# Performance work log

Hardware: AMD Instinct MI355X
Metric: run time of the kernel (lower is better)

## Reference

```python
import jax, jax.numpy as jnp
import numpy as np


def setup_inputs() -> dict:
    key = jax.random.key(0)
    ks = jax.random.split(key, 8)
    B, L, H, D = 128, 2048, 512, 512
    return {
        "batch": jax.random.normal(ks[0], (B, D), jnp.float32),
        "hid_states": jax.random.normal(ks[1], (B, L, H), jnp.float32),
        "h0": 0.1 * jax.random.normal(ks[2], (B, H), jnp.float32),
        "s0": 0.1 * jax.random.normal(ks[3], (B, H), jnp.float32),
        "W_ih": jax.random.normal(ks[4], (D, 4 * H), jnp.float32) * (1.0 / np.sqrt(D)),
        "W_hh": jax.random.normal(ks[5], (H, 4 * H), jnp.float32) * (1.0 / np.sqrt(H)),
        "b_lstm": jnp.zeros((4 * H,), jnp.float32),
        "W1": jax.random.normal(ks[6], (H, 64), jnp.float32) * (1.0 / np.sqrt(H)),
        "b1": jnp.zeros((64,), jnp.float32),
        "W2": jax.random.normal(ks[7], (64, D), jnp.float32) * (1.0 / np.sqrt(64)),
        "b2": jnp.zeros((D,), jnp.float32),
        "max_len": 10,
    }


def reference(batch, hid_states, h0, s0, W_ih, W_hh, b_lstm, W1, b1, W2, b2, max_len):
    B, D = batch.shape
    eps = 1e-8
    hs_sq = jnp.sum(hid_states * hid_states, axis=2)  # (B, L), loop-invariant

    def step(carry, _):
        x, h, s = carry
        # cosine-similarity attention of state s over recorded hidden states
        num = jnp.einsum('bh,blh->bl', s, hid_states)
        denom = jnp.sqrt(hs_sq * jnp.sum(s * s, axis=1, keepdims=True)) + eps
        energy = jax.nn.softmax(num / denom, axis=1)          # (B, L)
        context = jnp.einsum('blh,bl->bh', hid_states, energy)
        s = s + context
        # LSTM cell step (i, f, g, o gate order)
        gates = x @ W_ih + h @ W_hh + b_lstm
        i, f, g, o = jnp.split(gates, 4, axis=1)
        c = jax.nn.sigmoid(f) * s + jax.nn.sigmoid(i) * jnp.tanh(g)
        h = jax.nn.sigmoid(o) * jnp.tanh(c)
        # 2-layer MLP head produces next input
        x = jax.nn.leaky_relu(h @ W1 + b1, 0.01) @ W2 + b2
        return (x, h, c), x

    (_, _, _), outs = jax.lax.scan(step, (batch, h0, s0), None, length=max_len)
    # replicate torch: cat(dim=1) -> view(B, D, L) -> permute(0, 2, 1)
    flat = jnp.transpose(outs, (1, 0, 2)).reshape(B, max_len * D)
    return flat.reshape(B, D, max_len).transpose(0, 2, 1)
```

## Files before the change

### kernel.cpp

```cpp
#include <hip/hip_runtime.h>
#include <math.h>

#define B 128
#define L 2048
#define H 512
#define D 512
#define NG 2048
#define T 10
#define S 16
#define GB 256

#define OFF_S    ((size_t)0)
#define OFF_H    ((size_t)65536)
#define OFF_X    ((size_t)131072)
#define OFF_SS   ((size_t)196608)
#define OFF_G    ((size_t)196736)
#define OFF_PL   ((size_t)460928)
#define OFF_PCTX ((size_t)462976)
#define OFF_RN   ((size_t)1511552)
#define OFF_HB   ((size_t)1773696)

__device__ __forceinline__ float sigf(float x){ return 1.0f / (1.0f + __expf(-x)); }

__device__ __forceinline__ unsigned int b16r(float f){
    unsigned int u = __float_as_uint(f);
    return (u + 0x7FFFu + ((u >> 16) & 1u)) >> 16;
}
__device__ __forceinline__ unsigned int pack2(float lo, float hi){
    return b16r(lo) | (b16r(hi) << 16);
}

#define UNPK(u, f0, f1) { f0 = __uint_as_float((u) << 16); f1 = __uint_as_float((u) & 0xFFFF0000u); }

__device__ __forceinline__ float block_sum256(float v){
    for (int off = 32; off; off >>= 1) v += __shfl_xor(v, off, 64);
    __shared__ float r[4];
    int wave = threadIdx.x >> 6, lane = threadIdx.x & 63;
    if (lane == 0) r[wave] = v;
    __syncthreads();
    return r[0] + r[1] + r[2] + r[3];
}

__global__ void init_k(const float* __restrict__ s0, const float* __restrict__ h0,
                       const float* __restrict__ x0, float* __restrict__ ws){
    int b = blockIdx.x, t = threadIdx.x;
    float ssq = 0.f;
    for (int h = t; h < H; h += 256){
        float sv = s0[b*H + h];
        ws[OFF_S + b*H + h] = sv;
        ws[OFF_H + b*H + h] = h0[b*H + h];
        ssq += sv * sv;
    }
    for (int d = t; d < D; d += 256) ws[OFF_X + b*D + d] = x0[b*D + d];
    float tot = block_sum256(ssq);
    if (t == 0) ws[OFF_SS + b] = tot;
}

__device__ __forceinline__ void load_snorm(const float* __restrict__ ws, int b, int g, float* sf){
    const float* sb = ws + OFF_S + (size_t)b * H + g * 8;
    float rssb = rsqrtf(ws[OFF_SS + b]);
    #pragma unroll
    for (int cb = 0; cb < 4; cb++){
        float4 a = *(const float4*)(sb + cb*128);
        float4 c = *(const float4*)(sb + cb*128 + 4);
        sf[cb*8+0]=a.x*rssb; sf[cb*8+1]=a.y*rssb; sf[cb*8+2]=a.z*rssb; sf[cb*8+3]=a.w*rssb;
        sf[cb*8+4]=c.x*rssb; sf[cb*8+5]=c.y*rssb; sf[cb*8+6]=c.z*rssb; sf[cb*8+7]=c.w*rssb;
    }
}

__device__ __forceinline__ void attn_epilogue(float* ctx, float lsum, float* smem,
                                              float* __restrict__ ws, int b, int chunk,
                                              int wave, int g, int r){
    #pragma unroll
    for (int k = 0; k < 32; k++){
        ctx[k] += __shfl_xor(ctx[k], 16, 64);
        ctx[k] += __shfl_xor(ctx[k], 32, 64);
    }
    lsum += __shfl_xor(lsum, 16, 64);
    lsum += __shfl_xor(lsum, 32, 64);

    float (*lctx)[512] = (float(*)[512])smem;
    float* ll = smem + 2048;
    if (r == 0){
        #pragma unroll
        for (int cb = 0; cb < 4; cb++){
            float4 a = { ctx[cb*8+0], ctx[cb*8+1], ctx[cb*8+2], ctx[cb*8+3] };
            float4 c = { ctx[cb*8+4], ctx[cb*8+5], ctx[cb*8+6], ctx[cb*8+7] };
            *(float4*)&lctx[wave][cb*128 + g*8]     = a;
            *(float4*)&lctx[wave][cb*128 + g*8 + 4] = c;
        }
        if (g == 0) ll[wave] = lsum;
    }
    __syncthreads();
    int t = threadIdx.x;
    float* pc = ws + OFF_PCTX + ((size_t)b * S + chunk) * H;
    pc[t]       = lctx[0][t]     + lctx[1][t]     + lctx[2][t]     + lctx[3][t];
    pc[t + 256] = lctx[0][t+256] + lctx[1][t+256] + lctx[2][t+256] + lctx[3][t+256];
    if (t == 0) ws[OFF_PL + b*S + chunk] = ll[0] + ll[1] + ll[2] + ll[3];
}

__device__ __forceinline__ void attn_first_body(const float* __restrict__ hid,
                                                float* __restrict__ ws, int bid, float* smem){
    int b = bid >> 4, chunk = bid & (S - 1);
    int wave = threadIdx.x >> 6, lane = threadIdx.x & 63;
    int g = lane & 15, r = lane >> 4;
    float sf[32];
    load_snorm(ws, b, g, sf);

    int l0w = chunk * 128 + wave * 32;
    const float* hsrc = hid + ((size_t)b * L + l0w) * H + g * 8;
    uint4* hbdst = (uint4*)(ws + OFF_HB) + ((size_t)b * L + l0w) * 64 + g;
    float* rnw = ws + OFF_RN + (size_t)b * L + l0w;

    float ctx[32];
    #pragma unroll
    for (int k = 0; k < 32; k++) ctx[k] = 0.f;
    float lsum = 0.f;

    for (int it = 0; it < 8; it++){
        int ro = it*4 + r;
        const float* src = hsrc + (size_t)ro * H;
        float f[32];
        #pragma unroll
        for (int cb = 0; cb < 4; cb++){
            float4 a = *(const float4*)(src + cb*128);
            float4 c = *(const float4*)(src + cb*128 + 4);
            f[cb*8+0]=a.x; f[cb*8+1]=a.y; f[cb*8+2]=a.z; f[cb*8+3]=a.w;
            f[cb*8+4]=c.x; f[cb*8+5]=c.y; f[cb*8+6]=c.z; f[cb*8+7]=c.w;
        }
        float sq = 0.f, dot = 0.f;
        #pragma unroll
        for (int k = 0; k < 32; k++){ sq += f[k]*f[k]; dot += f[k]*sf[k]; }
        sq  += __shfl_xor(sq, 1, 64);  sq  += __shfl_xor(sq, 2, 64);
        sq  += __shfl_xor(sq, 4, 64);  sq  += __shfl_xor(sq, 8, 64);
        dot += __shfl_xor(dot, 1, 64); dot += __shfl_xor(dot, 2, 64);
        dot += __shfl_xor(dot, 4, 64); dot += __shfl_xor(dot, 8, 64);
        float rnv = rsqrtf(sq);
        if (g == 0) rnw[ro] = rnv;
        uint4* drow = hbdst + (size_t)ro * 64;
        #pragma unroll
        for (int cb = 0; cb < 4; cb++){
            uint4 o;
            o.x = pack2(f[cb*8+0], f[cb*8+1]);
            o.y = pack2(f[cb*8+2], f[cb*8+3]);
            o.z = pack2(f[cb*8+4], f[cb*8+5]);
            o.w = pack2(f[cb*8+6], f[cb*8+7]);
            drow[cb*16] = o;
        }
        float p = __expf(dot * rnv);
        lsum += p;
        #pragma unroll
        for (int k = 0; k < 32; k++) ctx[k] += p * f[k];
    }
    attn_epilogue(ctx, lsum, smem, ws, b, chunk, wave, g, r);
}

__device__ __forceinline__ void attn_steady_body(float* __restrict__ ws, int bid, float* smem){
    int b = bid >> 4, chunk = bid & (S - 1);
    int wave = threadIdx.x >> 6, lane = threadIdx.x & 63;
    int g = lane & 15, r = lane >> 4;
    float sf[32];
    load_snorm(ws, b, g, sf);

    int l0w = chunk * 128 + wave * 32;
    const uint4* hbu = (const uint4*)(ws + OFF_HB) + ((size_t)b * L + l0w) * 64 + g;
    const float* rnp = ws + OFF_RN + (size_t)b * L + l0w;

    float ctx[32];
    #pragma unroll
    for (int k = 0; k < 32; k++) ctx[k] = 0.f;
    float lsum = 0.f;

    for (int it = 0; it < 8; it++){
        int ro = it*4 + r;
        const uint4* hr = hbu + (size_t)ro * 64;
        uint4 u0 = hr[0];
        uint4 u1 = hr[16];
        uint4 u2 = hr[32];
        uint4 u3 = hr[48];
        float rnv = rnp[ro];
        float f[32];
        UNPK(u0.x, f[0], f[1])   UNPK(u0.y, f[2], f[3])
        UNPK(u0.z, f[4], f[5])   UNPK(u0.w, f[6], f[7])
        UNPK(u1.x, f[8], f[9])   UNPK(u1.y, f[10], f[11])
        UNPK(u1.z, f[12], f[13]) UNPK(u1.w, f[14], f[15])
        UNPK(u2.x, f[16], f[17]) UNPK(u2.y, f[18], f[19])
        UNPK(u2.z, f[20], f[21]) UNPK(u2.w, f[22], f[23])
        UNPK(u3.x, f[24], f[25]) UNPK(u3.y, f[26], f[27])
        UNPK(u3.z, f[28], f[29]) UNPK(u3.w, f[30], f[31])
        float dot = 0.f;
        #pragma unroll
        for (int k = 0; k < 32; k++) dot += f[k] * sf[k];
        dot += __shfl_xor(dot, 1, 64);
        dot += __shfl_xor(dot, 2, 64);
        dot += __shfl_xor(dot, 4, 64);
        dot += __shfl_xor(dot, 8, 64);
        float p = __expf(dot * rnv);
        lsum += p;
        #pragma unroll
        for (int k = 0; k < 32; k++) ctx[k] += p * f[k];
    }
    attn_epilogue(ctx, lsum, smem, ws, b, chunk, wave, g, r);
}

__device__ __forceinline__ void gates_body(const float* __restrict__ Wih,
                                           const float* __restrict__ Whh,
                                           const float* __restrict__ bias,
                                           float* __restrict__ ws,
                                           float* smem, int gid){
    int tid = threadIdx.x;
    int b0 = (gid >> 4) * 8, n0 = (gid & 15) * 128;
    float* xs  = smem;
    float* hsm = smem + 4096;
    {
        int r = tid >> 5, c = (tid & 31) * 16;
        const float* xsrc = ws + OFF_X + (size_t)(b0 + r) * D + c;
        const float* hsrc = ws + OFF_H + (size_t)(b0 + r) * H + c;
        #pragma unroll
        for (int j = 0; j < 4; j++){
            *(float4*)&xs[r*512 + c + j*4]  = *(const float4*)(xsrc + j*4);
            *(float4*)&hsm[r*512 + c + j*4] = *(const float4*)(hsrc + j*4);
        }
    }
    __syncthreads();
    int nt = tid & 31, kh = tid >> 5;
    int n = n0 + nt * 4;
    float4 acc[8];
    #pragma unroll
    for (int bi = 0; bi < 8; bi++){ acc[bi].x = 0.f; acc[bi].y = 0.f; acc[bi].z = 0.f; acc[bi].w = 0.f; }
    const float* w1p = Wih + (size_t)(kh * 64) * NG + n;
    const float* w2p = Whh + (size_t)(kh * 64) * NG + n;
    const float* xk = xs  + kh * 64;
    const float* hk = hsm + kh * 64;
    #pragma unroll 2
    for (int k = 0; k < 64; k++){
        float4 w1 = *(const float4*)(w1p + (size_t)k * NG);
        float4 w2 = *(const float4*)(w2p + (size_t)k * NG);
        #pragma unroll
        for (int bi = 0; bi < 8; bi++){
            float xv = xk[bi*512 + k], hv = hk[bi*512 + k];
            acc[bi].x += xv*w1.x + hv*w2.x;
            acc[bi].y += xv*w1.y + hv*w2.y;
            acc[bi].z += xv*w1.z + hv*w2.z;
            acc[bi].w += xv*w1.w + hv*w2.w;
        }
    }
    __syncthreads();
    float4* red = (float4*)smem;
    #pragma unroll
    for (int bi = 0; bi < 8; bi++) red[(kh*8 + bi)*32 + nt] = acc[bi];
    __syncthreads();
    int bi2 = tid >> 5, nt2 = tid & 31;
    int n2 = n0 + nt2 * 4;
    float4 s = *(const float4*)(bias + n2);
    #pragma unroll
    for (int k2 = 0; k2 < 8; k2++){
        float4 p = red[(k2*8 + bi2)*32 + nt2];
        s.x += p.x; s.y += p.y; s.z += p.z; s.w += p.w;
    }
    *(float4*)(ws + OFF_G + (size_t)(b0 + bi2)*NG + n2) = s;
}

__global__ __launch_bounds__(256, 3) void fused0_k(const float* __restrict__ hid,
                                                   const float* __restrict__ Wih,
                                                   const float* __restrict__ Whh,
                                                   const float* __restrict__ bias,
                                                   float* __restrict__ ws){
    __shared__ float smem[8192];
    if (blockIdx.x < GB){ gates_body(Wih, Whh, bias, ws, smem, blockIdx.x); return; }
    attn_first_body(hid, ws, blockIdx.x - GB, smem);
}

__global__ __launch_bounds__(256, 3) void fusedN_k(const float* __restrict__ Wih,
                                                   const float* __restrict__ Whh,
                                                   const float* __restrict__ bias,
                                                   float* __restrict__ ws){
    __shared__ float smem[8192];
    if (blockIdx.x < GB){ gates_body(Wih, Whh, bias, ws, smem, blockIdx.x); return; }
    attn_steady_body(ws, blockIdx.x - GB, smem);
}

__global__ __launch_bounds__(512) void tail_k(const float* __restrict__ W1, const float* __restrict__ b1,
                                              const float* __restrict__ W2, const float* __restrict__ b2,
                                              float* __restrict__ ws, float* __restrict__ out, int st){
    int b = blockIdx.x, t = threadIdx.x;
    __shared__ float hl[512];
    __shared__ float part[8][64];
    __shared__ float t1[64];
    __shared__ float rr[8];

    float Ls = 0.f;
    #pragma unroll
    for (int i = 0; i < S; i++) Ls += ws[OFF_PL + b*S + i];
    float inv = 1.0f / Ls;

    float cx = 0.f;
    #pragma unroll
    for (int i = 0; i < S; i++) cx += ws[OFF_PCTX + ((size_t)b*S + i)*H + t];
    const float* g = ws + OFF_G + (size_t)b * NG;
    float sn = ws[OFF_S + b*H + t] + cx * inv;
    float gi = g[t], gf = g[512 + t], gg = g[1024 + t], go = g[1536 + t];
    float c  = sigf(gf) * sn + sigf(gi) * tanhf(gg);
    float hv = sigf(go) * tanhf(c);
    ws[OFF_S + b*H + t] = c;
    ws[OFF_H + b*H + t] = hv;
    hl[t] = hv;
    float csq = c * c;
    for (int off = 32; off; off >>= 1) csq += __shfl_xor(csq, off, 64);
    int wv = t >> 6, ln = t & 63;
    if (ln == 0) rr[wv] = csq;
    __syncthreads();
    if (t == 0){
        float s = 0.f;
        #pragma unroll
        for (int i = 0; i < 8; i++) s += rr[i];
        ws[OFF_SS + b] = s;
    }

    int j = t & 63, q = t >> 6;
    float a = 0.f;
    #pragma unroll 4
    for (int k = q*64; k < q*64 + 64; k++) a += hl[k] * W1[k*64 + j];
    part[q][j] = a;
    __syncthreads();
    if (t < 64){
        float v = b1[t];
        #pragma unroll
        for (int i = 0; i < 8; i++) v += part[i][t];
        t1[t] = v > 0.f ? v : 0.01f * v;
    }
    __syncthreads();
    float a2 = b2[t];
    #pragma unroll
    for (int k = 0; k < 64; k++) a2 += t1[k] * W2[k*512 + t];
    ws[OFF_X + (size_t)b*D + t] = a2;
    int idx = st * D + t;
    out[(size_t)b * (D*T) + (size_t)(idx % T) * D + (idx / T)] = a2;
}

extern "C" void kernel_launch(void* const* d_in, const int* in_sizes, int n_in,
                              void* d_out, int out_size, void* d_ws, size_t ws_size,
                              hipStream_t stream) {
    const float* batch = (const float*)d_in[0];
    const float* hid   = (const float*)d_in[1];
    const float* h0    = (const float*)d_in[2];
    const float* s0    = (const float*)d_in[3];
    const float* Wih   = (const float*)d_in[4];
    const float* Whh   = (const float*)d_in[5];
    const float* bl    = (const float*)d_in[6];
    const float* W1    = (const float*)d_in[7];
    const float* b1    = (const float*)d_in[8];
    const float* W2    = (const float*)d_in[9];
    const float* b2    = (const float*)d_in[10];
    float* out = (float*)d_out;
    float* ws  = (float*)d_ws;

    init_k<<<B, 256, 0, stream>>>(s0, h0, batch, ws);
    fused0_k<<<B*S + GB, 256, 0, stream>>>(hid, Wih, Whh, bl, ws);
    tail_k<<<B, 512, 0, stream>>>(W1, b1, W2, b2, ws, out, 0);
    for (int st = 1; st < T; st++){
        fusedN_k<<<B*S + GB, 256, 0, stream>>>(Wih, Whh, bl, ws);
        tail_k<<<B, 512, 0, stream>>>(W1, b1, W2, b2, ws, out, st);
    }
}
```

Baseline: 1.419 ms.

## Remove init kernel, remap attention lanes to 32-wide rows with register prefetch

The separate init kernel is removed: step 0 reads s0, h0 and batch directly and computes the s-norm inside each attention block, while the tail kernel takes a pointer to the previous s. The attention loops now use 32 lanes per row with 16 elements each, so two rows are in flight per wave instead of four. The loops are fully unrolled with next-row prefetch into registers. Launch bounds are raised to 4 blocks per SM to increase occupancy, which adds register pressure from the prefetch buffers.

```diff
diff --git a/kernel.cpp b/kernel.cpp
--- a/kernel.cpp
+++ b/kernel.cpp
@@ -32,180 +32,193 @@
 
 #define UNPK(u, f0, f1) { f0 = __uint_as_float((u) << 16); f1 = __uint_as_float((u) & 0xFFFF0000u); }
 
-__device__ __forceinline__ float block_sum256(float v){
+__device__ __forceinline__ float red32(float v){
+    v += __shfl_xor(v, 1, 64);
+    v += __shfl_xor(v, 2, 64);
+    v += __shfl_xor(v, 4, 64);
+    v += __shfl_xor(v, 8, 64);
+    v += __shfl_xor(v, 16, 64);
+    return v;
+}
+
+__device__ __forceinline__ float block_sum256s(float v, float* r4){
     for (int off = 32; off; off >>= 1) v += __shfl_xor(v, off, 64);
-    __shared__ float r[4];
     int wave = threadIdx.x >> 6, lane = threadIdx.x & 63;
-    if (lane == 0) r[wave] = v;
-    __syncthreads();
-    return r[0] + r[1] + r[2] + r[3];
-}
-
-__global__ void init_k(const float* __restrict__ s0, const float* __restrict__ h0,
-                       const float* __restrict__ x0, float* __restrict__ ws){
-    int b = blockIdx.x, t = threadIdx.x;
-    float ssq = 0.f;
-    for (int h = t; h < H; h += 256){
-        float sv = s0[b*H + h];
-        ws[OFF_S + b*H + h] = sv;
-        ws[OFF_H + b*H + h] = h0[b*H + h];
-        ssq += sv * sv;
-    }
-    for (int d = t; d < D; d += 256) ws[OFF_X + b*D + d] = x0[b*D + d];
-    float tot = block_sum256(ssq);
-    if (t == 0) ws[OFF_SS + b] = tot;
-}
-
-__device__ __forceinline__ void load_snorm(const float* __restrict__ ws, int b, int g, float* sf){
-    const float* sb = ws + OFF_S + (size_t)b * H + g * 8;
-    float rssb = rsqrtf(ws[OFF_SS + b]);
-    #pragma unroll
-    for (int cb = 0; cb < 4; cb++){
-        float4 a = *(const float4*)(sb + cb*128);
-        float4 c = *(const float4*)(sb + cb*128 + 4);
-        sf[cb*8+0]=a.x*rssb; sf[cb*8+1]=a.y*rssb; sf[cb*8+2]=a.z*rssb; sf[cb*8+3]=a.w*rssb;
-        sf[cb*8+4]=c.x*rssb; sf[cb*8+5]=c.y*rssb; sf[cb*8+6]=c.z*rssb; sf[cb*8+7]=c.w*rssb;
-    }
-}
-
-__device__ __forceinline__ void attn_epilogue(float* ctx, float lsum, float* smem,
-                                              float* __restrict__ ws, int b, int chunk,
-                                              int wave, int g, int r){
-    #pragma unroll
-    for (int k = 0; k < 32; k++){
-        ctx[k] += __shfl_xor(ctx[k], 16, 64);
-        ctx[k] += __shfl_xor(ctx[k], 32, 64);
-    }
-    lsum += __shfl_xor(lsum, 16, 64);
+    if (lane == 0) r4[wave] = v;
+    __syncthreads();
+    return r4[0] + r4[1] + r4[2] + r4[3];
+}
+
+__device__ __forceinline__ void load_snorm16(const float* sptr, float rssb, int g2, float* sf){
+    const float* sb = sptr + g2 * 16;
+    #pragma unroll
+    for (int q = 0; q < 4; q++){
+        float4 a = *(const float4*)(sb + q*4);
+        sf[q*4+0] = a.x * rssb; sf[q*4+1] = a.y * rssb;
+        sf[q*4+2] = a.z * rssb; sf[q*4+3] = a.w * rssb;
+    }
+}
+
+__device__ __forceinline__ void attn_epilogue32(float* ctx, float lsum, float* smem,
+                                                float* __restrict__ pl, float* __restrict__ pc,
+                                                int wave, int g2, int lane){
+    #pragma unroll
+    for (int k = 0; k < 16; k++) ctx[k] += __shfl_xor(ctx[k], 32, 64);
     lsum += __shfl_xor(lsum, 32, 64);
 
     float (*lctx)[512] = (float(*)[512])smem;
     float* ll = smem + 2048;
-    if (r == 0){
-        #pragma unroll
-        for (int cb = 0; cb < 4; cb++){
-            float4 a = { ctx[cb*8+0], ctx[cb*8+1], ctx[cb*8+2], ctx[cb*8+3] };
-            float4 c = { ctx[cb*8+4], ctx[cb*8+5], ctx[cb*8+6], ctx[cb*8+7] };
-            *(float4*)&lctx[wave][cb*128 + g*8]     = a;
-            *(float4*)&lctx[wave][cb*128 + g*8 + 4] = c;
-        }
-        if (g == 0) ll[wave] = lsum;
+    if (lane < 32){
+        #pragma unroll
+        for (int q = 0; q < 4; q++){
+            float4 v = { ctx[q*4+0], ctx[q*4+1], ctx[q*4+2], ctx[q*4+3] };
+            *(float4*)&lctx[wave][g2*16 + q*4] = v;
+        }
+        if (g2 == 0) ll[wave] = lsum;
     }
     __syncthreads();
     int t = threadIdx.x;
-    float* pc = ws + OFF_PCTX + ((size_t)b * S + chunk) * H;
     pc[t]       = lctx[0][t]     + lctx[1][t]     + lctx[2][t]     + lctx[3][t];
     pc[t + 256] = lctx[0][t+256] + lctx[1][t+256] + lctx[2][t+256] + lctx[3][t+256];
-    if (t == 0) ws[OFF_PL + b*S + chunk] = ll[0] + ll[1] + ll[2] + ll[3];
+    if (t == 0) pl[0] = ll[0] + ll[1] + ll[2] + ll[3];
 }
 
 __device__ __forceinline__ void attn_first_body(const float* __restrict__ hid,
-                                                float* __restrict__ ws, int bid, float* smem){
-    int b = bid >> 4, chunk = bid & (S - 1);
+                                                const float* __restrict__ sptr, float rssb,
+                                                float* __restrict__ ws, float* smem,
+                                                float* __restrict__ pl, float* __restrict__ pc,
+                                                int b, int chunk){
     int wave = threadIdx.x >> 6, lane = threadIdx.x & 63;
-    int g = lane & 15, r = lane >> 4;
-    float sf[32];
-    load_snorm(ws, b, g, sf);
+    int g2 = lane & 31, r2 = lane >> 5;
+    float sf[16];
+    load_snorm16(sptr, rssb, g2, sf);
 
     int l0w = chunk * 128 + wave * 32;
-    const float* hsrc = hid + ((size_t)b * L + l0w) * H + g * 8;
-    uint4* hbdst = (uint4*)(ws + OFF_HB) + ((size_t)b * L + l0w) * 64 + g;
+    const float* hsrc = hid + ((size_t)b * L + l0w) * H + g2 * 16;
+    uint4* hbw = (uint4*)(ws + OFF_HB) + ((size_t)b * L + l0w) * 64 + g2 * 2;
     float* rnw = ws + OFF_RN + (size_t)b * L + l0w;
 
-    float ctx[32];
-    #pragma unroll
-    for (int k = 0; k < 32; k++) ctx[k] = 0.f;
+    float ctx[16];
+    #pragma unroll
+    for (int k = 0; k < 16; k++) ctx[k] = 0.f;
     float lsum = 0.f;
 
-    for (int it = 0; it < 8; it++){
-        int ro = it*4 + r;
-        const float* src = hsrc + (size_t)ro * H;
-        float f[32];
-        #pragma unroll
-        for (int cb = 0; cb < 4; cb++){
-            float4 a = *(const float4*)(src + cb*128);
-            float4 c = *(const float4*)(src + cb*128 + 4);
-            f[cb*8+0]=a.x; f[cb*8+1]=a.y; f[cb*8+2]=a.z; f[cb*8+3]=a.w;
-            f[cb*8+4]=c.x; f[cb*8+5]=c.y; f[cb*8+6]=c.z; f[cb*8+7]=c.w;
-        }
-        float sq = 0.f, dot = 0.f;
-        #pragma unroll
-        for (int k = 0; k < 32; k++){ sq += f[k]*f[k]; dot += f[k]*sf[k]; }
-        sq  += __shfl_xor(sq, 1, 64);  sq  += __shfl_xor(sq, 2, 64);
-        sq  += __shfl_xor(sq, 4, 64);  sq  += __shfl_xor(sq, 8, 64);
-        dot += __shfl_xor(dot, 1, 64); dot += __shfl_xor(dot, 2, 64);
-        dot += __shfl_xor(dot, 4, 64); dot += __shfl_xor(dot, 8, 64);
+    const float* s0p = hsrc + (size_t)r2 * H;
+    float4 x0 = *(const float4*)(s0p);
+    float4 x1 = *(const float4*)(s0p + 4);
+    float4 x2 = *(const float4*)(s0p + 8);
+    float4 x3 = *(const float4*)(s0p + 12);
+
+    #pragma unroll
+    for (int it = 0; it < 16; it++){
+        int ro = it*2 + r2;
+        float4 y0, y1, y2, y3;
+        if (it < 15){
+            const float* sn = hsrc + (size_t)(ro + 2) * H;
+            y0 = *(const float4*)(sn);
+            y1 = *(const float4*)(sn + 4);
+            y2 = *(const float4*)(sn + 8);
+            y3 = *(const float4*)(sn + 12);
+        }
+        float f[16];
+        f[0]=x0.x;  f[1]=x0.y;  f[2]=x0.z;  f[3]=x0.w;
+        f[4]=x1.x;  f[5]=x1.y;  f[6]=x1.z;  f[7]=x1.w;
+        f[8]=x2.x;  f[9]=x2.y;  f[10]=x2.z; f[11]=x2.w;
+        f[12]=x3.x; f[13]=x3.y; f[14]=x3.z; f[15]=x3.w;
+
+        float s0_=0.f, s1_=0.f, d0=0.f, d1=0.f, d2=0.f, d3=0.f;
+        #pragma unroll
+        for (int k = 0; k < 4; k++){
+            s0_ += f[k]*f[k] + f[4+k]*f[4+k];
+            s1_ += f[8+k]*f[8+k] + f[12+k]*f[12+k];
+            d0 += f[k]*sf[k];
+            d1 += f[4+k]*sf[4+k];
+            d2 += f[8+k]*sf[8+k];
+            d3 += f[12+k]*sf[12+k];
+        }
+        float sq  = red32(s0_ + s1_);
+        float dot = red32((d0 + d1) + (d2 + d3));
         float rnv = rsqrtf(sq);
-        if (g == 0) rnw[ro] = rnv;
-        uint4* drow = hbdst + (size_t)ro * 64;
-        #pragma unroll
-        for (int cb = 0; cb < 4; cb++){
-            uint4 o;
-            o.x = pack2(f[cb*8+0], f[cb*8+1]);
-            o.y = pack2(f[cb*8+2], f[cb*8+3]);
-            o.z = pack2(f[cb*8+4], f[cb*8+5]);
-            o.w = pack2(f[cb*8+6], f[cb*8+7]);
-            drow[cb*16] = o;
-        }
+        if (g2 == 0) rnw[ro] = rnv;
+
+        uint4 o0, o1;
+        o0.x = pack2(f[0], f[1]);   o0.y = pack2(f[2], f[3]);
+        o0.z = pack2(f[4], f[5]);   o0.w = pack2(f[6], f[7]);
+        o1.x = pack2(f[8], f[9]);   o1.y = pack2(f[10], f[11]);
+        o1.z = pack2(f[12], f[13]); o1.w = pack2(f[14], f[15]);
+        hbw[(size_t)ro * 64]     = o0;
+        hbw[(size_t)ro * 64 + 1] = o1;
+
         float p = __expf(dot * rnv);
         lsum += p;
         #pragma unroll
-        for (int k = 0; k < 32; k++) ctx[k] += p * f[k];
-    }
-    attn_epilogue(ctx, lsum, smem, ws, b, chunk, wave, g, r);
-}
-
-__device__ __forceinline__ void attn_steady_body(float* __restrict__ ws, int bid, float* smem){
-    int b = bid >> 4, chunk = bid & (S - 1);
+        for (int k = 0; k < 16; k++) ctx[k] += p * f[k];
+
+        if (it < 15){ x0 = y0; x1 = y1; x2 = y2; x3 = y3; }
+    }
+    attn_epilogue32(ctx, lsum, smem, pl, pc, wave, g2, lane);
+}
+
+__device__ __forceinline__ void attn_steady_body(const float* __restrict__ sptr, float rssb,
+                                                 const float* __restrict__ ws_c, float* smem,
+                                                 float* __restrict__ pl, float* __restrict__ pc,
+                                                 int b, int chunk){
     int wave = threadIdx.x >> 6, lane = threadIdx.x & 63;
-    int g = lane & 15, r = lane >> 4;
-    float sf[32];
-    load_snorm(ws, b, g, sf);
+    int g2 = lane & 31, r2 = lane >> 5;
+    float sf[16];
+    load_snorm16(sptr, rssb, g2, sf);
 
     int l0w = chunk * 128 + wave * 32;
-    const uint4* hbu = (const uint4*)(ws + OFF_HB) + ((size_t)b * L + l0w) * 64 + g;
-    const float* rnp = ws + OFF_RN + (size_t)b * L + l0w;
-
-    float ctx[32];
-    #pragma unroll
-    for (int k = 0; k < 32; k++) ctx[k] = 0.f;
+    const uint4* hbu = (const uint4*)(ws_c + OFF_HB) + ((size_t)b * L + l0w) * 64 + g2 * 2;
+    const float* rnp = ws_c + OFF_RN + (size_t)b * L + l0w;
+
+    float ctx[16];
+    #pragma unroll
+    for (int k = 0; k < 16; k++) ctx[k] = 0.f;
     float lsum = 0.f;
 
-    for (int it = 0; it < 8; it++){
-        int ro = it*4 + r;
-        const uint4* hr = hbu + (size_t)ro * 64;
-        uint4 u0 = hr[0];
-        uint4 u1 = hr[16];
-        uint4 u2 = hr[32];
-        uint4 u3 = hr[48];
-        float rnv = rnp[ro];
-        float f[32];
-        UNPK(u0.x, f[0], f[1])   UNPK(u0.y, f[2], f[3])
-        UNPK(u0.z, f[4], f[5])   UNPK(u0.w, f[6], f[7])
-        UNPK(u1.x, f[8], f[9])   UNPK(u1.y, f[10], f[11])
-        UNPK(u1.z, f[12], f[13]) UNPK(u1.w, f[14], f[15])
-        UNPK(u2.x, f[16], f[17]) UNPK(u2.y, f[18], f[19])
-        UNPK(u2.z, f[20], f[21]) UNPK(u2.w, f[22], f[23])
-        UNPK(u3.x, f[24], f[25]) UNPK(u3.y, f[26], f[27])
-        UNPK(u3.z, f[28], f[29]) UNPK(u3.w, f[30], f[31])
-        float dot = 0.f;
-        #pragma unroll
-        for (int k = 0; k < 32; k++) dot += f[k] * sf[k];
-        dot += __shfl_xor(dot, 1, 64);
-        dot += __shfl_xor(dot, 2, 64);
-        dot += __shfl_xor(dot, 4, 64);
-        dot += __shfl_xor(dot, 8, 64);
+    uint4 ua = hbu[(size_t)r2 * 64];
+    uint4 ub = hbu[(size_t)r2 * 64 + 1];
+    float rnv = rnp[r2];
+
+    #pragma unroll
+    for (int it = 0; it < 16; it++){
+        uint4 na, nb; float rnn;
+        if (it < 15){
+            const uint4* hn = hbu + (size_t)(it*2 + 2 + r2) * 64;
+            na = hn[0]; nb = hn[1];
+            rnn = rnp[it*2 + 2 + r2];
+        }
+        float f[16];
+        UNPK(ua.x, f[0],  f[1])   UNPK(ua.y, f[2],  f[3])
+        UNPK(ua.z, f[4],  f[5])   UNPK(ua.w, f[6],  f[7])
+        UNPK(ub.x, f[8],  f[9])   UNPK(ub.y, f[10], f[11])
+        UNPK(ub.z, f[12], f[13])  UNPK(ub.w, f[14], f[15])
+
+        float d0=0.f, d1=0.f, d2=0.f, d3=0.f;
+        #pragma unroll
+        for (int k = 0; k < 4; k++){
+            d0 += f[k]*sf[k];
+            d1 += f[4+k]*sf[4+k];
+            d2 += f[8+k]*sf[8+k];
+            d3 += f[12+k]*sf[12+k];
+        }
+        float dot = red32((d0 + d1) + (d2 + d3));
         float p = __expf(dot * rnv);
         lsum += p;
         #pragma unroll
-        for (int k = 0; k < 32; k++) ctx[k] += p * f[k];
-    }
-    attn_epilogue(ctx, lsum, smem, ws, b, chunk, wave, g, r);
+        for (int k = 0; k < 16; k++) ctx[k] += p * f[k];
+
+        if (it < 15){ ua = na; ub = nb; rnv = rnn; }
+    }
+    attn_epilogue32(ctx, lsum, smem, pl, pc, wave, g2, lane);
 }
 
 __device__ __forceinline__ void gates_body(const float* __restrict__ Wih,
                                            const float* __restrict__ Whh,
                                            const float* __restrict__ bias,
+                                           const float* __restrict__ xp,
+                                           const float* __restrict__ hp,
                                            float* __restrict__ ws,
                                            float* smem, int gid){
     int tid = threadIdx.x;
@@ -214,8 +227,8 @@
     float* hsm = smem + 4096;
     {
         int r = tid >> 5, c = (tid & 31) * 16;
-        const float* xsrc = ws + OFF_X + (size_t)(b0 + r) * D + c;
-        const float* hsrc = ws + OFF_H + (size_t)(b0 + r) * H + c;
+        const float* xsrc = xp + (size_t)(b0 + r) * D + c;
+        const float* hsrc = hp + (size_t)(b0 + r) * H + c;
         #pragma unroll
         for (int j = 0; j < 4; j++){
             *(float4*)&xs[r*512 + c + j*4]  = *(const float4*)(xsrc + j*4);
@@ -261,27 +274,48 @@
     *(float4*)(ws + OFF_G + (size_t)(b0 + bi2)*NG + n2) = s;
 }
 
-__global__ __launch_bounds__(256, 3) void fused0_k(const float* __restrict__ hid,
+__global__ __launch_bounds__(256, 4) void fused0_k(const float* __restrict__ hid,
+                                                   const float* __restrict__ batch,
+                                                   const float* __restrict__ h0,
+                                                   const float* __restrict__ s0,
                                                    const float* __restrict__ Wih,
                                                    const float* __restrict__ Whh,
                                                    const float* __restrict__ bias,
                                                    float* __restrict__ ws){
     __shared__ float smem[8192];
-    if (blockIdx.x < GB){ gates_body(Wih, Whh, bias, ws, smem, blockIdx.x); return; }
-    attn_first_body(hid, ws, blockIdx.x - GB, smem);
-}
-
-__global__ __launch_bounds__(256, 3) void fusedN_k(const float* __restrict__ Wih,
+    if (blockIdx.x < GB){ gates_body(Wih, Whh, bias, batch, h0, ws, smem, blockIdx.x); return; }
+    int bid = blockIdx.x - GB;
+    int b = bid >> 4, chunk = bid & (S - 1);
+    float ssq = 0.f;
+    int t = threadIdx.x;
+    {
+        float v0 = s0[(size_t)b*H + t];
+        float v1 = s0[(size_t)b*H + 256 + t];
+        ssq = v0*v0 + v1*v1;
+    }
+    float rssb = rsqrtf(block_sum256s(ssq, smem + 2052));
+    float* pl = ws + OFF_PL + b*S + chunk;
+    float* pc = ws + OFF_PCTX + ((size_t)(b*S + chunk))*H;
+    attn_first_body(hid, s0 + (size_t)b*H, rssb, ws, smem, pl, pc, b, chunk);
+}
+
+__global__ __launch_bounds__(256, 4) void fusedN_k(const float* __restrict__ Wih,
                                                    const float* __restrict__ Whh,
                                                    const float* __restrict__ bias,
                                                    float* __restrict__ ws){
     __shared__ float smem[8192];
-    if (blockIdx.x < GB){ gates_body(Wih, Whh, bias, ws, smem, blockIdx.x); return; }
-    attn_steady_body(ws, blockIdx.x - GB, smem);
+    if (blockIdx.x < GB){ gates_body(Wih, Whh, bias, ws + OFF_X, ws + OFF_H, ws, smem, blockIdx.x); return; }
+    int bid = blockIdx.x - GB;
+    int b = bid >> 4, chunk = bid & (S - 1);
+    float rssb = rsqrtf(ws[OFF_SS + b]);
+    float* pl = ws + OFF_PL + b*S + chunk;
+    float* pc = ws + OFF_PCTX + ((size_t)(b*S + chunk))*H;
+    attn_steady_body(ws + OFF_S + (size_t)b*H, rssb, ws, smem, pl, pc, b, chunk);
 }
 
 __global__ __launch_bounds__(512) void tail_k(const float* __restrict__ W1, const float* __restrict__ b1,
                                               const float* __restrict__ W2, const float* __restrict__ b2,
+                                              const float* __restrict__ sprev,
                                               float* __restrict__ ws, float* __restrict__ out, int st){
     int b = blockIdx.x, t = threadIdx.x;
     __shared__ float hl[512];
@@ -298,12 +332,12 @@
     #pragma unroll
     for (int i = 0; i < S; i++) cx += ws[OFF_PCTX + ((size_t)b*S + i)*H + t];
     const float* g = ws + OFF_G + (size_t)b * NG;
-    float sn = ws[OFF_S + b*H + t] + cx * inv;
+    float sn = sprev[(size_t)b*H + t] + cx * inv;
     float gi = g[t], gf = g[512 + t], gg = g[1024 + t], go = g[1536 + t];
     float c  = sigf(gf) * sn + sigf(gi) * tanhf(gg);
     float hv = sigf(go) * tanhf(c);
-    ws[OFF_S + b*H + t] = c;
-    ws[OFF_H + b*H + t] = hv;
+    ws[OFF_S + (size_t)b*H + t] = c;
+    ws[OFF_H + (size_t)b*H + t] = hv;
     hl[t] = hv;
     float csq = c * c;
     for (int off = 32; off; off >>= 1) csq += __shfl_xor(csq, off, 64);
@@ -355,11 +389,10 @@
     float* out = (float*)d_out;
     float* ws  = (float*)d_ws;
 
-    init_k<<<B, 256, 0, stream>>>(s0, h0, batch, ws);
-    fused0_k<<<B*S + GB, 256, 0, stream>>>(hid, Wih, Whh, bl, ws);
-    tail_k<<<B, 512, 0, stream>>>(W1, b1, W2, b2, ws, out, 0);
+    fused0_k<<<B*S + GB, 256, 0, stream>>>(hid, batch, h0, s0, Wih, Whh, bl, ws);
+    tail_k<<<B, 512, 0, stream>>>(W1, b1, W2, b2, s0, ws, out, 0);
     for (int st = 1; st < T; st++){
         fusedN_k<<<B*S + GB, 256, 0, stream>>>(Wih, Whh, bl, ws);
-        tail_k<<<B, 512, 0, stream>>>(W1, b1, W2, b2, ws, out, st);
-    }
-}
+        tail_k<<<B, 512, 0, stream>>>(W1, b1, W2, b2, ws + OFF_S, ws, out, st);
+    }
+}
```

New measurement: 3.472 ms. +144.7%, slower.
